# Kernel optimization log

Hardware: AMD Instinct MI355X
Metric: run time of the kernel (lower is better)

The kernel has to match this reference:

```python
import jax, jax.numpy as jnp
import numpy as np

B = 4096   # batch
V = 512    # num_variables
H = 64     # hidden_dim


def setup_inputs() -> dict:
    key = jax.random.key(0)
    ks = jax.random.split(key, 6)
    return {
        "X": jax.random.normal(ks[0], (B, V), dtype=jnp.float32),
        "adjacency_logits": jax.random.normal(ks[1], (V, V), dtype=jnp.float32) * 0.1,
        # W1[i] is the first Linear of net i: maps V inputs -> H hidden
        "W1": jax.random.normal(ks[2], (V, V, H), dtype=jnp.float32) * (1.0 / np.sqrt(V)),
        "b1": jax.random.normal(ks[3], (V, H), dtype=jnp.float32) * 0.01,
        # W2[i] is the second Linear of net i: maps H hidden -> 1 output
        "W2": jax.random.normal(ks[4], (V, H), dtype=jnp.float32) * (1.0 / np.sqrt(H)),
        "b2": jax.random.normal(ks[5], (V,), dtype=jnp.float32) * 0.01,
    }


def reference(X, adjacency_logits, W1, b1, W2, b2):
    # Hard adjacency (hard_adjacency=True path): threshold sigmoid, zero diagonal.
    probs = jax.nn.sigmoid(adjacency_logits)
    adj = (probs > 0.5).astype(X.dtype) * (1.0 - jnp.eye(V, dtype=X.dtype))  # [V, V]

    # Original loop: for each i, net_i(X * adj[:, i]).
    # Fold the parent mask into the first-layer weights: W1_eff[i, v, h] = W1[i, v, h] * adj[v, i]
    W1_eff = W1 * adj.T[:, :, None]                      # [V, V, H]
    h = jax.nn.relu(jnp.einsum('bv,ivh->bih', X, W1_eff) + b1[None])  # [B, V, H]
    reconstructed = jnp.einsum('bih,ih->bi', h, W2) + b2[None]        # [B, V]
    return reconstructed, adj
```

## Files before the change

kernel.cpp:

```cpp
#include <hip/hip_runtime.h>
#include <hip/hip_bf16.h>
#include <stdint.h>

#define BB 4096
#define VV 512
#define HH 64

typedef short bf16x8 __attribute__((ext_vector_type(8)));
typedef float floatx4 __attribute__((ext_vector_type(4)));
typedef unsigned short ushort8 __attribute__((ext_vector_type(8)));

typedef const __attribute__((address_space(1))) void g_void;
typedef __attribute__((address_space(3))) void l_void;

__device__ __forceinline__ void gload_lds16(const void* g, void* l) {
    __builtin_amdgcn_global_load_lds((g_void*)g, (l_void*)l, 16, 0, 0);
}

__device__ __forceinline__ unsigned short f2bf_rne(float f) {
    unsigned int u = __float_as_uint(f);
    u += 0x7FFFu + ((u >> 16) & 1u);
    return (unsigned short)(u >> 16);
}

__global__ __launch_bounds__(256) void adj_kernel(const float* __restrict__ logits,
                                                  float* __restrict__ adj_out) {
    int idx = blockIdx.x * 256 + threadIdx.x;
    int v = idx >> 9, u = idx & (VV - 1);
    adj_out[idx] = (logits[idx] > 0.0f && v != u) ? 1.0f : 0.0f;
}

__global__ __launch_bounds__(256) void prep_fused_kernel(
        const float* __restrict__ X, const float* __restrict__ logits,
        const float* __restrict__ W1, float* __restrict__ adj_out,
        unsigned short* __restrict__ Xp, unsigned short* __restrict__ W1t) {
    __shared__ float tile[64][65];
    __shared__ float maskv[64];
    int bx = blockIdx.x;
    int t  = threadIdx.x;
    if (bx < 4096) {
        int i  = bx >> 3;
        int v0 = (bx & 7) << 6;
        if (t < 64) {
            int v = v0 + t;
            maskv[t] = (logits[(size_t)v * VV + i] > 0.0f && v != i) ? 1.0f : 0.0f;
        }
        const float4* src4 = (const float4*)(W1 + ((size_t)i * VV + v0) * HH);
        #pragma unroll
        for (int jj = 0; jj < 4; ++jj) {
            int c  = jj * 256 + t;
            int vr = c >> 4, h4 = c & 15;
            float4 w = src4[c];
            tile[vr][h4 * 4 + 0] = w.x;
            tile[vr][h4 * 4 + 1] = w.y;
            tile[vr][h4 * 4 + 2] = w.z;
            tile[vr][h4 * 4 + 3] = w.w;
        }
        __syncthreads();
        unsigned short* dst = W1t + (size_t)i * (HH * VV) + v0;
        #pragma unroll
        for (int j = 0; j < 2; ++j) {
            int c = j * 256 + t;
            int h = c >> 3;
            int vr0 = (c & 7) * 8;
            ushort8 o;
            #pragma unroll
            for (int r = 0; r < 8; ++r)
                o[r] = f2bf_rne(tile[vr0 + r][h] * maskv[vr0 + r]);
            *(ushort8*)&dst[(size_t)h * VV + vr0] = o;
        }
    } else {
        int idx = (bx - 4096) * 256 + t;
        {
            int v = idx >> 9, u = idx & (VV - 1);
            adj_out[idx] = (logits[idx] > 0.0f && v != u) ? 1.0f : 0.0f;
        }
        {
            int lane = idx & 63;
            int mt   = (idx >> 6) & 3;
            int ks   = (idx >> 8) & 15;
            int rb   = idx >> 12;
            int row  = rb * 64 + mt * 16 + (lane & 15);
            int k0   = ks * 32 + (lane >> 4) * 8;
            const float4* s4 = (const float4*)(X + (size_t)row * VV + k0);
            float4 a = s4[0], b = s4[1];
            ushort8 o;
            o[0] = f2bf_rne(a.x); o[1] = f2bf_rne(a.y);
            o[2] = f2bf_rne(a.z); o[3] = f2bf_rne(a.w);
            o[4] = f2bf_rne(b.x); o[5] = f2bf_rne(b.y);
            o[6] = f2bf_rne(b.z); o[7] = f2bf_rne(b.w);
            *(ushort8*)(Xp + (size_t)idx * 8) = o;
        }
    }
}

__global__ __launch_bounds__(256, 2) void dag_gemm_kernel(
        const unsigned short* __restrict__ Xp,
        const unsigned short* __restrict__ W1t,
        const float* __restrict__ b1,
        const float* __restrict__ W2,
        const float* __restrict__ b2,
        float* __restrict__ out)
{
    __shared__ __align__(16) unsigned short Ws[2][16384];
    __shared__ float Po[2][256];

    const int t    = threadIdx.x;
    const int wave = t >> 6;
    const int lane = t & 63;
    const int ln   = lane & 15;
    const int quad = lane >> 4;

    const int bx   = blockIdx.x;
    const int i0   = (bx >> 4) << 1;
    const int row0 = (bx & 15) << 8;

    auto ldb = [&](int ii, int pos, int nt) -> bf16x8 {
        return *(const bf16x8*)&Ws[ii][(nt * 16 + ln) * 256 + ((pos ^ (ln & 7)) * 8)];
    };

    const unsigned short* abase =
        Xp + (size_t)((row0 >> 6) + wave) * (64 * VV) + lane * 8;

    bf16x8 af[2][4];
    #pragma unroll
    for (int mt = 0; mt < 4; ++mt)
        af[0][mt] = *(const bf16x8*)(abase + mt * 512);

    const unsigned short* wb0 = W1t + (size_t)i0 * (HH * VV);
    const unsigned short* wb1 = W1t + (size_t)(i0 + 1) * (HH * VV);
    auto stage = [&](int kb) {
        #pragma unroll
        for (int j = 0; j < 8; ++j) {
            int c = j * 256 + t;
            int h = c >> 5, s2 = c & 31;
            size_t off = (size_t)h * VV + (size_t)(kb + (s2 ^ (h & 7))) * 8;
            gload_lds16(wb0 + off, (char*)&Ws[0][0] + c * 16);
            gload_lds16(wb1 + off, (char*)&Ws[1][0] + c * 16);
        }
    };
    stage(0);
    __syncthreads();

    floatx4 acc[2][4][4];
    #pragma unroll
    for (int ii = 0; ii < 2; ++ii)
        #pragma unroll
        for (int a = 0; a < 4; ++a)
            #pragma unroll
            for (int b = 0; b < 4; ++b)
                acc[ii][a][b] = (floatx4){0.f, 0.f, 0.f, 0.f};

    bf16x8 bq[2][2][4];
    #pragma unroll
    for (int ii = 0; ii < 2; ++ii)
        #pragma unroll
        for (int nt = 0; nt < 4; ++nt)
            bq[0][ii][nt] = ldb(ii, quad, nt);

    #pragma unroll
    for (int kk = 0; kk < 8; ++kk) {
        #pragma unroll
        for (int mt = 0; mt < 4; ++mt)
            af[(kk + 1) & 1][mt] =
                *(const bf16x8*)(abase + ((kk + 1) * 4 + mt) * 512);
        if (kk < 7) {
            #pragma unroll
            for (int ii = 0; ii < 2; ++ii)
                #pragma unroll
                for (int nt = 0; nt < 4; ++nt)
                    bq[(kk + 1) & 1][ii][nt] = ldb(ii, (kk + 1) * 4 + quad, nt);
        }
        #pragma unroll
        for (int ii = 0; ii < 2; ++ii)
            #pragma unroll
            for (int mt = 0; mt < 4; ++mt)
                #pragma unroll
                for (int nt = 0; nt < 4; ++nt)
                    acc[ii][mt][nt] = __builtin_amdgcn_mfma_f32_16x16x32_bf16(
                        af[kk & 1][mt], bq[kk & 1][ii][nt], acc[ii][mt][nt], 0, 0, 0);
    }

    __syncthreads();

    stage(32);
    __syncthreads();

    #pragma unroll
    for (int ii = 0; ii < 2; ++ii)
        #pragma unroll
        for (int nt = 0; nt < 4; ++nt)
            bq[0][ii][nt] = ldb(ii, quad, nt);

    #pragma unroll
    for (int kk = 8; kk < 16; ++kk) {
        if (kk < 15) {
            #pragma unroll
            for (int mt = 0; mt < 4; ++mt)
                af[(kk + 1) & 1][mt] =
                    *(const bf16x8*)(abase + ((kk + 1) * 4 + mt) * 512);
            #pragma unroll
            for (int ii = 0; ii < 2; ++ii)
                #pragma unroll
                for (int nt = 0; nt < 4; ++nt)
                    bq[(kk + 1) & 1][ii][nt] = ldb(ii, ((kk + 1) - 8) * 4 + quad, nt);
        }
        #pragma unroll
        for (int ii = 0; ii < 2; ++ii)
            #pragma unroll
            for (int mt = 0; mt < 4; ++mt)
                #pragma unroll
                for (int nt = 0; nt < 4; ++nt)
                    acc[ii][mt][nt] = __builtin_amdgcn_mfma_f32_16x16x32_bf16(
                        af[kk & 1][mt], bq[kk & 1][ii][nt], acc[ii][mt][nt], 0, 0, 0);
    }

    float b1v[2][4], w2v[2][4], b2i[2];
    #pragma unroll
    for (int ii = 0; ii < 2; ++ii) {
        #pragma unroll
        for (int nt = 0; nt < 4; ++nt) {
            b1v[ii][nt] = b1[(i0 + ii) * HH + nt * 16 + ln];
            w2v[ii][nt] = W2[(i0 + ii) * HH + nt * 16 + ln];
        }
        b2i[ii] = b2[i0 + ii];
    }
    #pragma unroll
    for (int ii = 0; ii < 2; ++ii) {
        #pragma unroll
        for (int mt = 0; mt < 4; ++mt) {
            #pragma unroll
            for (int r = 0; r < 4; ++r) {
                float p = 0.f;
                #pragma unroll
                for (int nt = 0; nt < 4; ++nt) {
                    float hv = acc[ii][mt][nt][r] + b1v[ii][nt];
                    hv = hv > 0.f ? hv : 0.f;
                    p += hv * w2v[ii][nt];
                }
                p += __shfl_xor(p, 8);
                p += __shfl_xor(p, 4);
                p += __shfl_xor(p, 2);
                p += __shfl_xor(p, 1);
                if (ln == 0)
                    Po[ii][wave * 64 + mt * 16 + quad * 4 + r] = p + b2i[ii];
            }
        }
    }
    const int row = row0 + wave * 64 + lane;
    out[(size_t)row * VV + i0]     = Po[0][wave * 64 + lane];
    out[(size_t)row * VV + i0 + 1] = Po[1][wave * 64 + lane];
}

__global__ __launch_bounds__(256) void fallback_kernel(
        const float* __restrict__ X, const float* __restrict__ logits,
        const float* __restrict__ W1, const float* __restrict__ b1,
        const float* __restrict__ W2, const float* __restrict__ b2,
        float* __restrict__ out) {
    __shared__ float Wc[128][64];
    int i   = blockIdx.x & (VV - 1);
    int row = (blockIdx.x >> 9) * 256 + threadIdx.x;
    float acc[64];
    #pragma unroll
    for (int h = 0; h < 64; ++h) acc[h] = 0.f;
    for (int v0 = 0; v0 < VV; v0 += 128) {
        __syncthreads();
        for (int j = 0; j < 32; ++j) {
            int idx = j * 256 + threadIdx.x;
            int vr = idx >> 6, h = idx & 63;
            int v = v0 + vr;
            float m = (logits[(size_t)v * VV + i] > 0.f && v != i) ? 1.f : 0.f;
            Wc[vr][h] = W1[((size_t)i * VV + v) * HH + h] * m;
        }
        __syncthreads();
        for (int vr = 0; vr < 128; ++vr) {
            float xv = X[(size_t)row * VV + v0 + vr];
            #pragma unroll
            for (int h = 0; h < 64; ++h) acc[h] += xv * Wc[vr][h];
        }
    }
    float p = b2[i];
    #pragma unroll
    for (int h = 0; h < 64; ++h) {
        float hv = acc[h] + b1[i * HH + h];
        p += (hv > 0.f ? hv : 0.f) * W2[i * HH + h];
    }
    out[(size_t)row * VV + i] = p;
}

extern "C" void kernel_launch(void* const* d_in, const int* in_sizes, int n_in,
                              void* d_out, int out_size, void* d_ws, size_t ws_size,
                              hipStream_t stream) {
    const float* X      = (const float*)d_in[0];
    const float* logits = (const float*)d_in[1];
    const float* W1     = (const float*)d_in[2];
    const float* b1     = (const float*)d_in[3];
    const float* W2     = (const float*)d_in[4];
    const float* b2     = (const float*)d_in[5];

    float* out     = (float*)d_out;
    float* adj_out = out + (size_t)BB * VV;

    const size_t xp_bytes  = (size_t)BB * VV * 2;
    const size_t w1t_bytes = (size_t)VV * HH * VV * 2;
    const size_t need = xp_bytes + w1t_bytes;

    if (ws_size >= need) {
        unsigned short* Xp  = (unsigned short*)d_ws;
        unsigned short* W1t = (unsigned short*)((char*)d_ws + xp_bytes);
        hipLaunchKernelGGL(prep_fused_kernel, dim3(5120), dim3(256), 0, stream,
                           X, logits, W1, adj_out, Xp, W1t);
        hipLaunchKernelGGL(dag_gemm_kernel, dim3(4096), dim3(256), 0, stream,
                           Xp, W1t, b1, W2, b2, out);
    } else {
        hipLaunchKernelGGL(adj_kernel, dim3((VV * VV) / 256), dim3(256), 0, stream,
                           logits, adj_out);
        hipLaunchKernelGGL(fallback_kernel, dim3(VV * (BB / 256)), dim3(256), 0, stream,
                           X, logits, W1, b1, W2, b2, out);
    }
}
```

Before: 244.6 us.

## Pipeline W1 tiles through a triple-buffered LDS ring with fine-grained waits

Replaces the two-phase load of W1 (two half-K stages, each fully synchronized) with an 8-step loop over 64-wide K tiles held in a 3-slot LDS ring. Each tile is prefetched two steps ahead using direct global-to-LDS loads, and explicit s_waitcnt vmcnt and s_barrier calls replace __syncthreads. MFMA blocks are wrapped in s_setprio to favor matrix issue. The aim is to hide global load latency behind compute instead of stalling at the stage boundary. In exchange it relies on hand-counted vmcnt values, which also include the A-fragment global loads, so miscounting could cause races.

```diff
diff --git a/kernel.cpp b/kernel.cpp
--- a/kernel.cpp
+++ b/kernel.cpp
@@ -102,12 +102,12 @@
         const float* __restrict__ b2,
         float* __restrict__ out)
 {
-    __shared__ __align__(16) unsigned short Ws[2][16384];
+    __shared__ __align__(16) unsigned short Ws[3 * 8192];
     __shared__ float Po[2][256];
 
-    const int t    = threadIdx.x;
-    const int wave = t >> 6;
-    const int lane = t & 63;
+    const int tid  = threadIdx.x;
+    const int wave = tid >> 6;
+    const int lane = tid & 63;
     const int ln   = lane & 15;
     const int quad = lane >> 4;
 
@@ -115,8 +115,21 @@
     const int i0   = (bx >> 4) << 1;
     const int row0 = (bx & 15) << 8;
 
-    auto ldb = [&](int ii, int pos, int nt) -> bf16x8 {
-        return *(const bf16x8*)&Ws[ii][(nt * 16 + ln) * 256 + ((pos ^ (ln & 7)) * 8)];
+    const unsigned short* wb0 = W1t + (size_t)i0 * (HH * VV);
+    auto stage = [&](int tt, int buf) {
+        #pragma unroll
+        for (int j = 0; j < 4; ++j) {
+            int c = j * 256 + tid;
+            int ii = c >> 9, h = (c >> 3) & 63, s = c & 7;
+            gload_lds16(wb0 + (size_t)ii * (HH * VV) + h * VV + tt * 64
+                            + ((s ^ (h & 7)) * 8),
+                        (char*)Ws + buf * 16384 + c * 16);
+        }
+    };
+
+    auto ldb = [&](const unsigned short* wb, int ii, int pos, int nt) -> bf16x8 {
+        return *(const bf16x8*)&wb[ii * 4096 + (nt * 16 + ln) * 64
+                                   + ((pos ^ (ln & 7)) * 8)];
     };
 
     const unsigned short* abase =
@@ -126,21 +139,10 @@
     #pragma unroll
     for (int mt = 0; mt < 4; ++mt)
         af[0][mt] = *(const bf16x8*)(abase + mt * 512);
-
-    const unsigned short* wb0 = W1t + (size_t)i0 * (HH * VV);
-    const unsigned short* wb1 = W1t + (size_t)(i0 + 1) * (HH * VV);
-    auto stage = [&](int kb) {
-        #pragma unroll
-        for (int j = 0; j < 8; ++j) {
-            int c = j * 256 + t;
-            int h = c >> 5, s2 = c & 31;
-            size_t off = (size_t)h * VV + (size_t)(kb + (s2 ^ (h & 7))) * 8;
-            gload_lds16(wb0 + off, (char*)&Ws[0][0] + c * 16);
-            gload_lds16(wb1 + off, (char*)&Ws[1][0] + c * 16);
-        }
-    };
-    stage(0);
-    __syncthreads();
+    stage(0, 0);
+    stage(1, 1);
+    asm volatile("s_waitcnt vmcnt(4)" ::: "memory");
+    asm volatile("s_barrier" ::: "memory");
 
     floatx4 acc[2][4][4];
     #pragma unroll
@@ -152,25 +154,26 @@
                 acc[ii][a][b] = (floatx4){0.f, 0.f, 0.f, 0.f};
 
     bf16x8 bq[2][2][4];
-    #pragma unroll
-    for (int ii = 0; ii < 2; ++ii)
-        #pragma unroll
-        for (int nt = 0; nt < 4; ++nt)
-            bq[0][ii][nt] = ldb(ii, quad, nt);
-
-    #pragma unroll
-    for (int kk = 0; kk < 8; ++kk) {
+
+    #pragma unroll
+    for (int tt = 0; tt < 8; ++tt) {
+        const unsigned short* wb = Ws + (tt % 3) * 8192;
+
+        #pragma unroll
+        for (int ii = 0; ii < 2; ++ii)
+            #pragma unroll
+            for (int nt = 0; nt < 4; ++nt)
+                bq[0][ii][nt] = ldb(wb, ii, quad, nt);
         #pragma unroll
         for (int mt = 0; mt < 4; ++mt)
-            af[(kk + 1) & 1][mt] =
-                *(const bf16x8*)(abase + ((kk + 1) * 4 + mt) * 512);
-        if (kk < 7) {
-            #pragma unroll
-            for (int ii = 0; ii < 2; ++ii)
-                #pragma unroll
-                for (int nt = 0; nt < 4; ++nt)
-                    bq[(kk + 1) & 1][ii][nt] = ldb(ii, (kk + 1) * 4 + quad, nt);
-        }
+            af[1][mt] = *(const bf16x8*)(abase + ((2 * tt + 1) * 4 + mt) * 512);
+        #pragma unroll
+        for (int ii = 0; ii < 2; ++ii)
+            #pragma unroll
+            for (int nt = 0; nt < 4; ++nt)
+                bq[1][ii][nt] = ldb(wb, ii, 4 + quad, nt);
+
+        __builtin_amdgcn_s_setprio(1);
         #pragma unroll
         for (int ii = 0; ii < 2; ++ii)
             #pragma unroll
@@ -178,33 +181,16 @@
                 #pragma unroll
                 for (int nt = 0; nt < 4; ++nt)
                     acc[ii][mt][nt] = __builtin_amdgcn_mfma_f32_16x16x32_bf16(
-                        af[kk & 1][mt], bq[kk & 1][ii][nt], acc[ii][mt][nt], 0, 0, 0);
-    }
-
-    __syncthreads();
-
-    stage(32);
-    __syncthreads();
-
-    #pragma unroll
-    for (int ii = 0; ii < 2; ++ii)
-        #pragma unroll
-        for (int nt = 0; nt < 4; ++nt)
-            bq[0][ii][nt] = ldb(ii, quad, nt);
-
-    #pragma unroll
-    for (int kk = 8; kk < 16; ++kk) {
-        if (kk < 15) {
+                        af[0][mt], bq[0][ii][nt], acc[ii][mt][nt], 0, 0, 0);
+        __builtin_amdgcn_s_setprio(0);
+
+        if (tt < 7) {
             #pragma unroll
             for (int mt = 0; mt < 4; ++mt)
-                af[(kk + 1) & 1][mt] =
-                    *(const bf16x8*)(abase + ((kk + 1) * 4 + mt) * 512);
-            #pragma unroll
-            for (int ii = 0; ii < 2; ++ii)
-                #pragma unroll
-                for (int nt = 0; nt < 4; ++nt)
-                    bq[(kk + 1) & 1][ii][nt] = ldb(ii, ((kk + 1) - 8) * 4 + quad, nt);
-        }
+                af[0][mt] = *(const bf16x8*)(abase + ((2 * tt + 2) * 4 + mt) * 512);
+        }
+
+        __builtin_amdgcn_s_setprio(1);
         #pragma unroll
         for (int ii = 0; ii < 2; ++ii)
             #pragma unroll
@@ -212,7 +198,16 @@
                 #pragma unroll
                 for (int nt = 0; nt < 4; ++nt)
                     acc[ii][mt][nt] = __builtin_amdgcn_mfma_f32_16x16x32_bf16(
-                        af[kk & 1][mt], bq[kk & 1][ii][nt], acc[ii][mt][nt], 0, 0, 0);
+                        af[1][mt], bq[1][ii][nt], acc[ii][mt][nt], 0, 0, 0);
+        __builtin_amdgcn_s_setprio(0);
+
+        if (tt < 6) stage(tt + 2, (tt + 2) % 3);
+
+        if (tt < 7) {
+            if (tt < 6) asm volatile("s_waitcnt vmcnt(12)" ::: "memory");
+            else        asm volatile("s_waitcnt vmcnt(8)"  ::: "memory");
+            asm volatile("s_barrier" ::: "memory");
+        }
     }
 
     float b1v[2][4], w2v[2][4], b2i[2];
```

Result: no change. 242.4 us (-0.9%).

## Double-buffer W1 transpose tiles and coalesce X reads in prep kernel

Applied to the files above, without the earlier changes.

The W1 mask-transpose part of the prep kernel now has each block handle four 64-row tiles (256 v values) with a double-buffered LDS tile, so the global load of the next tile overlaps the conversion and store of the current one. Grid size drops from 5120 to 2048 blocks. The X bf16 packing now reads X row-contiguously and scatters writes into the MFMA-friendly packed layout, instead of gathering reads. This trades fewer blocks, and possibly lower parallelism in the prep stage, for better memory coalescing and load/store overlap.

```diff
diff --git a/kernel.cpp b/kernel.cpp
--- a/kernel.cpp
+++ b/kernel.cpp
@@ -34,54 +34,63 @@
         const float* __restrict__ X, const float* __restrict__ logits,
         const float* __restrict__ W1, float* __restrict__ adj_out,
         unsigned short* __restrict__ Xp, unsigned short* __restrict__ W1t) {
-    __shared__ float tile[64][65];
-    __shared__ float maskv[64];
+    __shared__ float tile[2][64][65];
+    __shared__ float maskv[256];
     int bx = blockIdx.x;
     int t  = threadIdx.x;
-    if (bx < 4096) {
-        int i  = bx >> 3;
-        int v0 = (bx & 7) << 6;
-        if (t < 64) {
+    if (bx < 1024) {
+        int i  = bx >> 1;
+        int v0 = (bx & 1) << 8;
+        {
             int v = v0 + t;
             maskv[t] = (logits[(size_t)v * VV + i] > 0.0f && v != i) ? 1.0f : 0.0f;
         }
         const float4* src4 = (const float4*)(W1 + ((size_t)i * VV + v0) * HH);
-        #pragma unroll
-        for (int jj = 0; jj < 4; ++jj) {
-            int c  = jj * 256 + t;
-            int vr = c >> 4, h4 = c & 15;
-            float4 w = src4[c];
-            tile[vr][h4 * 4 + 0] = w.x;
-            tile[vr][h4 * 4 + 1] = w.y;
-            tile[vr][h4 * 4 + 2] = w.z;
-            tile[vr][h4 * 4 + 3] = w.w;
-        }
+        unsigned short* dst0 = W1t + (size_t)i * (HH * VV) + v0;
+
+        auto load = [&](int s, int b) {
+            #pragma unroll
+            for (int jj = 0; jj < 4; ++jj) {
+                int c  = jj * 256 + t;
+                int vr = c >> 4, h4 = c & 15;
+                float4 w = src4[s * 1024 + c];
+                tile[b][vr][h4 * 4 + 0] = w.x;
+                tile[b][vr][h4 * 4 + 1] = w.y;
+                tile[b][vr][h4 * 4 + 2] = w.z;
+                tile[b][vr][h4 * 4 + 3] = w.w;
+            }
+        };
+        auto store = [&](int s, int b) {
+            #pragma unroll
+            for (int j = 0; j < 2; ++j) {
+                int c = j * 256 + t;
+                int h = c >> 3;
+                int vr0 = (c & 7) * 8;
+                ushort8 o;
+                #pragma unroll
+                for (int r = 0; r < 8; ++r)
+                    o[r] = f2bf_rne(tile[b][vr0 + r][h] * maskv[s * 64 + vr0 + r]);
+                *(ushort8*)&dst0[(size_t)h * VV + s * 64 + vr0] = o;
+            }
+        };
+
+        load(0, 0);
         __syncthreads();
-        unsigned short* dst = W1t + (size_t)i * (HH * VV) + v0;
-        #pragma unroll
-        for (int j = 0; j < 2; ++j) {
-            int c = j * 256 + t;
-            int h = c >> 3;
-            int vr0 = (c & 7) * 8;
-            ushort8 o;
-            #pragma unroll
-            for (int r = 0; r < 8; ++r)
-                o[r] = f2bf_rne(tile[vr0 + r][h] * maskv[vr0 + r]);
-            *(ushort8*)&dst[(size_t)h * VV + vr0] = o;
+        #pragma unroll
+        for (int s = 0; s < 4; ++s) {
+            if (s < 3) load(s + 1, (s + 1) & 1);
+            store(s, s & 1);
+            __syncthreads();
         }
     } else {
-        int idx = (bx - 4096) * 256 + t;
+        int idx = (bx - 1024) * 256 + t;
         {
             int v = idx >> 9, u = idx & (VV - 1);
             adj_out[idx] = (logits[idx] > 0.0f && v != u) ? 1.0f : 0.0f;
         }
         {
-            int lane = idx & 63;
-            int mt   = (idx >> 6) & 3;
-            int ks   = (idx >> 8) & 15;
-            int rb   = idx >> 12;
-            int row  = rb * 64 + mt * 16 + (lane & 15);
-            int k0   = ks * 32 + (lane >> 4) * 8;
+            int row = idx >> 6;
+            int k0  = (idx & 63) << 3;
             const float4* s4 = (const float4*)(X + (size_t)row * VV + k0);
             float4 a = s4[0], b = s4[1];
             ushort8 o;
@@ -89,7 +98,10 @@
             o[2] = f2bf_rne(a.z); o[3] = f2bf_rne(a.w);
             o[4] = f2bf_rne(b.x); o[5] = f2bf_rne(b.y);
             o[6] = f2bf_rne(b.z); o[7] = f2bf_rne(b.w);
-            *(ushort8*)(Xp + (size_t)idx * 8) = o;
+            int rb = row >> 6, mt = (row >> 4) & 3, lnr = row & 15;
+            int ks = k0 >> 5, quad = (k0 >> 3) & 3;
+            size_t chunk = (((size_t)(rb * 16 + ks) * 4 + mt) << 6) + quad * 16 + lnr;
+            *(ushort8*)(Xp + chunk * 8) = o;
         }
     }
 }
@@ -308,7 +320,7 @@
     if (ws_size >= need) {
         unsigned short* Xp  = (unsigned short*)d_ws;
         unsigned short* W1t = (unsigned short*)((char*)d_ws + xp_bytes);
-        hipLaunchKernelGGL(prep_fused_kernel, dim3(5120), dim3(256), 0, stream,
+        hipLaunchKernelGGL(prep_fused_kernel, dim3(2048), dim3(256), 0, stream,
                            X, logits, W1, adj_out, Xp, W1t);
         hipLaunchKernelGGL(dag_gemm_kernel, dim3(4096), dim3(256), 0, stream,
                            Xp, W1t, b1, W2, b2, out);
```

Result: faster. 239.2 us (median of 3 runs) (-2.2%).
